# Kernel tuning notes

Hardware: AMD Instinct MI355X
Metric: run time of the kernel (lower is better)

The kernel has to match this reference:

```python
import jax, jax.numpy as jnp
import numpy as np

IMG_H = IMG_W = 2048
N_LEVELS = 16
N_FEAT = 2
LOG2_T = 19
T = 1 << LOG2_T  # 524288 hash table entries per level
BASE = 16.0
FINEST = 2048.0
P1 = np.uint32(2654435761)  # second spatial-hash prime (first prime is 1)
MASK = np.uint32(T - 1)
OFFSETS = jnp.array([[0, 0], [0, 1], [1, 0], [1, 1]], dtype=jnp.int32)


def _resolutions():
    # matches torch float32 arithmetic: b = exp((ln finest - ln base)/(L-1))
    b = np.float32(np.exp((np.log(np.float32(FINEST)) - np.log(np.float32(BASE))) / (N_LEVELS - 1)))
    return [int(np.floor(np.float32(BASE) * b ** np.float32(i))) for i in range(N_LEVELS)]

RES = _resolutions()


def _sorted_vertex_hashes(res):
    # hash_integer over the full (res+1)x(res+1) vertex grid, sorted -> the consistent-hash ring.
    g = np.arange(res + 1, dtype=np.uint32)
    h = (g[:, None] ^ (g[None, :] * P1)) & MASK  # uint32 wraps, low 19 bits identical to int64 torch
    return np.sort(h.ravel()).astype(np.int32)

# Only levels whose dense grid exceeds the hash table use consistent hashing.
SORTED = {i: jnp.asarray(_sorted_vertex_hashes(RES[i]))
          for i in range(N_LEVELS) if (RES[i] + 1) ** 2 > T}


def setup_inputs() -> dict:
    key = jax.random.key(0)
    k1, k2 = jax.random.split(key)
    B = 1 << 21  # ~2.1M query points
    x = jax.random.uniform(k1, (B, 2), dtype=jnp.float32) * jnp.array([IMG_H, IMG_W], jnp.float32)
    tables = jax.random.uniform(k2, (N_LEVELS, T, N_FEAT), dtype=jnp.float32,
                                minval=-1e-4, maxval=1e-4)
    return {"x": x, "tables": tables}


def _level_embed(x, table, level):
    res = RES[level]
    gs = jnp.array([IMG_H / res, IMG_W / res], jnp.float32)  # [y_grid_size, x_grid_size]
    bl = jnp.floor(x / gs).astype(jnp.int32)                 # bottom-left cell index, [B,2]
    gmin = bl.astype(jnp.float32) * gs
    gmax = gmin + gs
    corners = bl[:, None, :] + OFFSETS[None]                 # [B,4,2] four cell corners
    if (res + 1) ** 2 <= T:
        idx = corners[..., 0] * res + corners[..., 1]        # one-to-one hash
    else:
        # spatial hash, then consistent-hash ring lookup. The torch code adds a
        # fractional hash in (0,1) and searches radian keys (h'+1)*delta; since all
        # keys/queries are integer grid hashes this reduces exactly to: first table
        # entry >= h (and h is always present, so value == h pre-densify).
        h = ((corners[..., 0].astype(jnp.uint32)
              ^ (corners[..., 1].astype(jnp.uint32) * P1)) & MASK).astype(jnp.int32)
        tab = SORTED[level]
        idx = tab[jnp.searchsorted(tab, h)]                  # [B,4]
    emb = table[idx]                                         # [B,4,F] gather
    w = (x - gmin) / (gmax - gmin)                           # bilinear weights, [B,2]
    w0 = w[:, 0:1]
    w1 = w[:, 1:2]
    c0 = emb[:, 0] * (1 - w1) + emb[:, 1] * w1
    c1 = emb[:, 2] * (1 - w1) + emb[:, 3] * w1
    return c0 * (1 - w0) + c1 * w0                           # [B,F]


def reference(x, tables):
    outs = [_level_embed(x, tables[i], i) for i in range(N_LEVELS)]
    return jnp.concatenate(outs, axis=-1)                    # [B, N_LEVELS*N_FEAT]
```

## Files before the change

kernel.cpp:

```cpp
#include <hip/hip_runtime.h>
#include <cstdint>

#define TSIZE (1u << 19)
#define MASKU (TSIZE - 1u)
#define P1U 2654435761u

#define CBINS_X 128
#define NCHILD (CBINS_X * CBINS_X)
#define XPART 8
#define CAPX 32
#define SLOTS (XPART * NCHILD * CAPX)

__device__ __forceinline__ void embed_point(float2 xv, int orig,
                                            const float* __restrict__ tables,
                                            float* __restrict__ out) {
  constexpr int RESV[16] = {16, 22, 30, 42, 58, 80, 111, 153,
                            212, 294, 406, 561, 776, 1072, 1482, 2047};
  const float2* tabs = reinterpret_cast<const float2*>(tables);

  float4 lo[12], hi[12];
  float2 eh[4][4];
  float w0a[16], w1a[16];

#pragma unroll
  for (int l = 0; l < 12; ++l) {
    const int res = RESV[l];
    const float gs = (float)(2048.0 / (double)res);
    float f0 = floorf(xv.x / gs);
    float f1 = floorf(xv.y / gs);
    float g0 = f0 * gs;
    float g1 = f1 * gs;
    w0a[l] = (xv.x - g0) / ((g0 + gs) - g0);
    w1a[l] = (xv.y - g1) / ((g1 + gs) - g1);
    int base = (int)f0 * res + (int)f1;
    const float2* tab = tabs + (size_t)l * TSIZE;
    lo[l] = *reinterpret_cast<const float4*>(tab + base);
    hi[l] = *reinterpret_cast<const float4*>(tab + base + res);
  }
#pragma unroll
  for (int l = 0; l < 4; ++l) {
    const int res = RESV[12 + l];
    const float gs = (float)(2048.0 / (double)res);
    float f0 = floorf(xv.x / gs);
    float f1 = floorf(xv.y / gs);
    float g0 = f0 * gs;
    float g1 = f1 * gs;
    w0a[12 + l] = (xv.x - g0) / ((g0 + gs) - g0);
    w1a[12 + l] = (xv.y - g1) / ((g1 + gs) - g1);
    uint32_t u0 = (uint32_t)(int)f0;
    uint32_t u1m = (uint32_t)(int)f1 * P1U;
    const float2* tab = tabs + (size_t)(12 + l) * TSIZE;
    eh[l][0] = tab[(u0 ^ u1m) & MASKU];
    eh[l][1] = tab[(u0 ^ (u1m + P1U)) & MASKU];
    eh[l][2] = tab[((u0 + 1u) ^ u1m) & MASKU];
    eh[l][3] = tab[((u0 + 1u) ^ (u1m + P1U)) & MASKU];
  }

  float feat[32];
#pragma unroll
  for (int l = 0; l < 12; ++l) {
    float w0 = w0a[l], w1 = w1a[l];
    float omw0 = 1.0f - w0, omw1 = 1.0f - w1;
    float c0x = lo[l].x * omw1 + lo[l].z * w1;
    float c0y = lo[l].y * omw1 + lo[l].w * w1;
    float c1x = hi[l].x * omw1 + hi[l].z * w1;
    float c1y = hi[l].y * omw1 + hi[l].w * w1;
    feat[2 * l]     = c0x * omw0 + c1x * w0;
    feat[2 * l + 1] = c0y * omw0 + c1y * w0;
  }
#pragma unroll
  for (int l = 0; l < 4; ++l) {
    float w0 = w0a[12 + l], w1 = w1a[12 + l];
    float omw0 = 1.0f - w0, omw1 = 1.0f - w1;
    float c0x = eh[l][0].x * omw1 + eh[l][1].x * w1;
    float c0y = eh[l][0].y * omw1 + eh[l][1].y * w1;
    float c1x = eh[l][2].x * omw1 + eh[l][3].x * w1;
    float c1y = eh[l][2].y * omw1 + eh[l][3].y * w1;
    feat[24 + 2 * l]     = c0x * omw0 + c1x * w0;
    feat[24 + 2 * l + 1] = c0y * omw0 + c1y * w0;
  }

  float4* o = reinterpret_cast<float4*>(out) + (size_t)orig * 8;
#pragma unroll
  for (int j = 0; j < 8; ++j) {
    o[j] = make_float4(feat[4 * j], feat[4 * j + 1], feat[4 * j + 2], feat[4 * j + 3]);
  }
}


__device__ __forceinline__ int child_of(float2 xv) {
  int bx = min((int)(xv.x * 0.0625f), CBINS_X - 1);
  int by = min((int)(xv.y * 0.0625f), CBINS_X - 1);
  int parent = ((bx >> 1) << 6) + (by >> 1);
  int quad = ((bx & 1) << 1) + (by & 1);
  return (parent << 2) + quad;
}

__global__ __launch_bounds__(256) void scatter_px(
    const float2* __restrict__ xs, int* __restrict__ cnt,
    float4* __restrict__ recs,
    int* __restrict__ ovf, int* __restrict__ ovf_cnt, int B) {
  int p = blockIdx.x * 256 + threadIdx.x;
  if (p >= B) return;
  int part = blockIdx.x & 7;
  float2 xv = xs[p];
  int pc = part * NCHILD + child_of(xv);
  int pos = atomicAdd(&cnt[pc], 1);
  if (pos < CAPX) {
    recs[(size_t)pc * CAPX + pos] =
        make_float4(xv.x, xv.y, __int_as_float(p), 0.0f);
  } else {
    int o = atomicAdd(ovf_cnt, 1);
    ovf[o] = p;
  }
}

__global__ __launch_bounds__(256, 2) void hashenc_cmp(
    const float4* __restrict__ recs, const int* __restrict__ cnt,
    const float* __restrict__ tables, float* __restrict__ out) {
  __shared__ int pre[9];
  int bid = blockIdx.x;
  int nb = gridDim.x;
  int chunk = nb >> 3;
  int child = (bid & 7) * chunk + (bid >> 3);
  if (threadIdx.x == 0) {
    int s = 0;
    pre[0] = 0;
#pragma unroll
    for (int k = 0; k < XPART; ++k) {
      s += min(cnt[k * NCHILD + child], CAPX);
      pre[k + 1] = s;
    }
  }
  __syncthreads();
  int total = pre[8];
  int i = threadIdx.x;
  if (i >= total) return;
  int k = 0;
#pragma unroll
  for (int kk = 1; kk < XPART; ++kk) k = (i >= pre[kk]) ? kk : k;
  int j = i - pre[k];
  float4 r = recs[((size_t)(k * NCHILD + child)) * CAPX + j];
  embed_point(make_float2(r.x, r.y), __float_as_int(r.z), tables, out);
}

__global__ __launch_bounds__(256) void ovf_kernel(
    const float2* __restrict__ xs, const int* __restrict__ ovf,
    const int* __restrict__ ovf_cnt, const float* __restrict__ tables,
    float* __restrict__ out) {
  int n = *ovf_cnt;
  for (int i = blockIdx.x * 256 + threadIdx.x; i < n; i += gridDim.x * 256) {
    int p = ovf[i];
    embed_point(xs[p], p, tables, out);
  }
}


__global__ __launch_bounds__(256, 2) void hashenc_plain(
    const float2* __restrict__ xs, const float* __restrict__ tables,
    float* __restrict__ out, int B) {
  int p = blockIdx.x * 256 + threadIdx.x;
  if (p >= B) return;
  embed_point(xs[p], p, tables, out);
}


extern "C" void kernel_launch(void* const* d_in, const int* in_sizes, int n_in,
                              void* d_out, int out_size, void* d_ws, size_t ws_size,
                              hipStream_t stream) {
  const float2* xs = (const float2*)d_in[0];
  const float* tables = (const float*)d_in[1];
  float* out = (float*)d_out;
  int B = in_sizes[0] / 2;
  int blocks = (B + 255) / 256;
  char* ws = (char*)d_ws;

  size_t c_recs = 0;
  size_t c_ovf = c_recs + (size_t)SLOTS * 16;
  size_t c_cnt = c_ovf + (size_t)B * 4;
  size_t c_ocnt = c_cnt + (size_t)XPART * NCHILD * 4;
  size_t need = c_ocnt + 64;

  bool grid_ok = (blocks & 7) == 0;
  if (grid_ok && ws_size >= need) {
    float4* recs = (float4*)(ws + c_recs);
    int* ovf = (int*)(ws + c_ovf);
    int* cnt = (int*)(ws + c_cnt);
    int* ovf_cnt = (int*)(ws + c_ocnt);
    (void)hipMemsetAsync(cnt, 0, (size_t)XPART * NCHILD * 4 + 64, stream);
    hipLaunchKernelGGL(scatter_px, dim3(blocks), dim3(256), 0, stream,
                       xs, cnt, recs, ovf, ovf_cnt, B);
    hipLaunchKernelGGL(hashenc_cmp, dim3(NCHILD), dim3(256), 0, stream,
                       recs, cnt, tables, out);
    hipLaunchKernelGGL(ovf_kernel, dim3(32), dim3(256), 0, stream,
                       xs, ovf, ovf_cnt, tables, out);
  } else {
    hipLaunchKernelGGL(hashenc_plain, dim3(blocks), dim3(256), 0, stream,
                       xs, tables, out, B);
  }
}
```

Measured before the change: 277.5 us.

## Process four sibling child bins per block in the compute kernel

The compute kernel now assigns one parent cell (four quadrant child bins across all eight partitions) to each block instead of a single child bin, launching a quarter as many blocks. Each thread handles up to four points through a shared-memory bin map built from a 32-entry prefix sum. The aim is fewer, fuller blocks (each previous block had only ~128 points for 256 threads) and better cache locality across neighbouring cells. The cost is a serial bin-map fill by 32 threads, an extra barrier, and a per-thread loop over points that may reduce latency hiding.

```diff
diff --git a/kernel.cpp b/kernel.cpp
--- a/kernel.cpp
+++ b/kernel.cpp
@@ -7,6 +7,7 @@
 
 #define CBINS_X 128
 #define NCHILD (CBINS_X * CBINS_X)
+#define NPAR (NCHILD / 4)
 #define XPART 8
 #define CAPX 32
 #define SLOTS (XPART * NCHILD * CAPX)
@@ -115,33 +116,46 @@
   }
 }
 
-__global__ __launch_bounds__(256, 2) void hashenc_cmp(
+__global__ __launch_bounds__(256, 2) void hashenc_par(
     const float4* __restrict__ recs, const int* __restrict__ cnt,
     const float* __restrict__ tables, float* __restrict__ out) {
-  __shared__ int pre[9];
+  __shared__ int pre[33];
+  __shared__ short bmap[1024];
   int bid = blockIdx.x;
   int nb = gridDim.x;
   int chunk = nb >> 3;
-  int child = (bid & 7) * chunk + (bid >> 3);
+  int par = (bid & 7) * chunk + (bid >> 3);
+
   if (threadIdx.x == 0) {
     int s = 0;
     pre[0] = 0;
 #pragma unroll
-    for (int k = 0; k < XPART; ++k) {
-      s += min(cnt[k * NCHILD + child], CAPX);
-      pre[k + 1] = s;
+    for (int b = 0; b < 32; ++b) {
+      int c = b >> 3, k = b & 7;
+      s += min(cnt[k * NCHILD + (par * 4 + c)], CAPX);
+      pre[b + 1] = s;
     }
   }
   __syncthreads();
-  int total = pre[8];
-  int i = threadIdx.x;
-  if (i >= total) return;
-  int k = 0;
-#pragma unroll
-  for (int kk = 1; kk < XPART; ++kk) k = (i >= pre[kk]) ? kk : k;
-  int j = i - pre[k];
-  float4 r = recs[((size_t)(k * NCHILD + child)) * CAPX + j];
-  embed_point(make_float2(r.x, r.y), __float_as_int(r.z), tables, out);
+  if (threadIdx.x < 32) {
+    int b = threadIdx.x;
+    int s = pre[b], e = pre[b + 1];
+    for (int j = s; j < e; ++j) bmap[j] = (short)b;
+  }
+  __syncthreads();
+
+  int total = pre[32];
+#pragma unroll
+  for (int rep = 0; rep < 4; ++rep) {
+    int idx = threadIdx.x + rep * 256;
+    if (idx < total) {
+      int b = bmap[idx];
+      int c = b >> 3, k = b & 7;
+      int j = idx - pre[b];
+      float4 r = recs[((size_t)(k * NCHILD + par * 4 + c)) * CAPX + j];
+      embed_point(make_float2(r.x, r.y), __float_as_int(r.z), tables, out);
+    }
+  }
 }
 
 __global__ __launch_bounds__(256) void ovf_kernel(
@@ -190,7 +204,7 @@
     (void)hipMemsetAsync(cnt, 0, (size_t)XPART * NCHILD * 4 + 64, stream);
     hipLaunchKernelGGL(scatter_px, dim3(blocks), dim3(256), 0, stream,
                        xs, cnt, recs, ovf, ovf_cnt, B);
-    hipLaunchKernelGGL(hashenc_cmp, dim3(NCHILD), dim3(256), 0, stream,
+    hipLaunchKernelGGL(hashenc_par, dim3(NPAR), dim3(256), 0, stream,
                        recs, cnt, tables, out);
     hipLaunchKernelGGL(ovf_kernel, dim3(32), dim3(256), 0, stream,
                        xs, ovf, ovf_cnt, tables, out);
```

Measured after the change: 282.2 us. About the same (+1.7%).
